# Performance work log

Hardware: AMD Instinct MI355X
Metric: run time of the kernel (lower is better)

Reference implementation:

```python
import jax, jax.numpy as jnp
import numpy as np


def _sage_layer(x, src, dst, W_self, W_neigh, b, n_nodes):
    # mean aggregation over incoming edges: agg[v] = mean(x[u] for (u,v) in E)
    agg = jax.ops.segment_sum(x[src], dst, num_segments=n_nodes)          # [N, D]
    cnt = jax.ops.segment_sum(jnp.ones((src.shape[0],), x.dtype), dst,
                              num_segments=n_nodes)                        # [N]
    agg = agg / jnp.clip(cnt, 1.0)[:, None]
    # h = ReLU(x W_self^T + agg W_neigh^T + b)   (torch Linear weight is [out, in])
    h = jnp.einsum('nd,od->no', x, W_self) + jnp.einsum('nd,od->no', agg, W_neigh) + b
    return jax.nn.relu(h)


def setup_inputs() -> dict:
    key = jax.random.key(0)
    ks = jax.random.split(key, 7)
    N, E = 50000, 800000
    F_IN, H, F_OUT = 128, 256, 128
    x = jax.random.normal(ks[0], (N, F_IN), dtype=jnp.float32)
    edge_index = jax.random.randint(ks[1], (2, E), 0, N, dtype=jnp.int64)
    s = 0.05
    return {
        'x': x,
        'edge_index': edge_index,
        'W_self1': jax.random.normal(ks[2], (H, F_IN), dtype=jnp.float32) * s,
        'W_neigh1': jax.random.normal(ks[3], (H, F_IN), dtype=jnp.float32) * s,
        'b1': jnp.zeros((H,), dtype=jnp.float32),
        'W_self2': jax.random.normal(ks[4], (F_OUT, H), dtype=jnp.float32) * s,
        'W_neigh2': jax.random.normal(ks[5], (F_OUT, H), dtype=jnp.float32) * s,
        'b2': jnp.zeros((F_OUT,), dtype=jnp.float32),
    }


def reference(x, edge_index, W_self1, W_neigh1, b1, W_self2, W_neigh2, b2):
    n_nodes = x.shape[0]
    src, dst = edge_index[0], edge_index[1]
    h = _sage_layer(x, src, dst, W_self1, W_neigh1, b1, n_nodes)
    # dropout is identity at inference
    h = _sage_layer(h, src, dst, W_self2, W_neigh2, b2, n_nodes)
    return h
```

## Files before the change

### kernel.cpp

```cpp
#include <hip/hip_runtime.h>


#define CAP 64
#define CPAD 16
#define NSLICE 8

typedef __attribute__((ext_vector_type(8))) short bfrag;
typedef __attribute__((ext_vector_type(4))) float ffrag;

__device__ inline unsigned short f2bf(float f) {
    union { float f; unsigned u; } v; v.f = f;
    unsigned r = (v.u + 0x7FFFu + ((v.u >> 16) & 1u)) >> 16;
    return (unsigned short)r;
}

__global__ __launch_bounds__(256) void prep_kernel(
        const int* __restrict__ src, const int* __restrict__ dst,
        int* __restrict__ cnt, unsigned short* __restrict__ adj,
        int E, int nper, int nfill,
        const float* __restrict__ x, unsigned short* __restrict__ xb, long xn4,
        int xblocks,
        const float* __restrict__ W0, const float* __restrict__ W1,
        const float* __restrict__ W2, const float* __restrict__ W3,
        unsigned short* __restrict__ O0, unsigned short* __restrict__ O1,
        unsigned short* __restrict__ O2, unsigned short* __restrict__ O3)
{
    int b = blockIdx.x;
    if (b < nfill) {
        int slice = b & (NSLICE - 1);
        int e = (b >> 3) * 256 + (int)threadIdx.x;
        if (e >= E) return;
        int d = dst[e];
        if ((unsigned)(d - slice * nper) >= (unsigned)nper) return;
        int s = src[e];
        int r = atomicAdd(&cnt[d * CPAD], 1);
        if (r < CAP) adj[(size_t)d * CAP + r] = (unsigned short)s;
        return;
    }
    b -= nfill;
    if (b < xblocks) {
        long i = (long)b * 256 + threadIdx.x;
        if (i >= xn4) return;
        float4 v = *(const float4*)(x + i * 4);
        ushort4 o;
        o.x = f2bf(v.x); o.y = f2bf(v.y); o.z = f2bf(v.z); o.w = f2bf(v.w);
        *(ushort4*)(xb + i * 4) = o;
        return;
    }
    b -= xblocks;
    int i = b * 256 + (int)threadIdx.x;
    int sel = i >> 13, off = i & 8191;
    const float* srcw = (sel == 0) ? W0 : (sel == 1) ? W1 : (sel == 2) ? W2 : W3;
    unsigned short* dstw = (sel == 0) ? O0 : (sel == 1) ? O1 : (sel == 2) ? O2 : O3;
    float4 v = ((const float4*)srcw)[off];
    ushort4 o;
    o.x = f2bf(v.x); o.y = f2bf(v.y); o.z = f2bf(v.z); o.w = f2bf(v.w);
    ((ushort4*)dstw)[off] = o;
}

#define BFLO(u) __uint_as_float((u) << 16)
#define BFHI(u) __uint_as_float((u) & 0xFFFF0000u)

#define ACC8(V)  do {                                                          \
    acc0 += BFLO(V.x); acc1 += BFHI(V.x); acc2 += BFLO(V.y); acc3 += BFHI(V.y);\
    acc4 += BFLO(V.z); acc5 += BFHI(V.z); acc6 += BFLO(V.w); acc7 += BFHI(V.w);\
} while (0)

__global__ __launch_bounds__(256, 2) void fused_l1(
        const unsigned short* __restrict__ xbu, const int* __restrict__ cnt,
        const unsigned short* __restrict__ adj,
        const short* __restrict__ Ws, const short* __restrict__ Wn,
        const float* __restrict__ bias, unsigned short* __restrict__ h1b, int NT)
{
    const short* xb = (const short*)xbu;
    const int wave = threadIdx.x >> 6, lane = threadIdx.x & 63;
    const int ln = lane & 15, lk = lane >> 4;
    const int gn = threadIdx.x >> 4;
    const int sp = threadIdx.x & 15;

    __shared__ unsigned short aggT[16][136];

    bfrag wfs[4][4], wfn[4][4];
    #pragma unroll
    for (int m = 0; m < 4; ++m) {
        const short* ws = Ws + (size_t)((wave * 4 + m) * 16 + ln) * 128 + lk * 8;
        const short* wn = Wn + (size_t)((wave * 4 + m) * 16 + ln) * 128 + lk * 8;
        #pragma unroll
        for (int kc = 0; kc < 4; ++kc) {
            wfs[m][kc] = *(const bfrag*)(ws + kc * 32);
            wfn[m][kc] = *(const bfrag*)(wn + kc * 32);
        }
    }
    float4 bv[4];
    #pragma unroll
    for (int m = 0; m < 4; ++m)
        bv[m] = *(const float4*)(bias + (wave * 4 + m) * 16 + lk * 4);

    for (int nt = blockIdx.x; nt < NT; nt += gridDim.x) {
        {
            int node = nt * 16 + gn;
            int c = cnt[node * CPAD]; if (c > CAP) c = CAP;
            const unsigned short* al = adj + (size_t)node * CAP;
            float acc0 = 0.f, acc1 = 0.f, acc2 = 0.f, acc3 = 0.f;
            float acc4 = 0.f, acc5 = 0.f, acc6 = 0.f, acc7 = 0.f;
            int j = 0;
            for (; j + 3 < c; j += 4) {
                ushort4 q = *(const ushort4*)(al + j);
                uint4 v0 = *(const uint4*)(xbu + (size_t)q.x * 128 + sp * 8);
                uint4 v1 = *(const uint4*)(xbu + (size_t)q.y * 128 + sp * 8);
                uint4 v2 = *(const uint4*)(xbu + (size_t)q.z * 128 + sp * 8);
                uint4 v3 = *(const uint4*)(xbu + (size_t)q.w * 128 + sp * 8);
                ACC8(v0); ACC8(v1); ACC8(v2); ACC8(v3);
            }
            for (; j < c; ++j) {
                uint4 v = *(const uint4*)(xbu + (size_t)al[j] * 128 + sp * 8);
                ACC8(v);
            }
            float s = (c > 0) ? 1.0f / (float)c : 0.0f;
            uint4 o;
            o.x = (unsigned)f2bf(acc0 * s) | ((unsigned)f2bf(acc1 * s) << 16);
            o.y = (unsigned)f2bf(acc2 * s) | ((unsigned)f2bf(acc3 * s) << 16);
            o.z = (unsigned)f2bf(acc4 * s) | ((unsigned)f2bf(acc5 * s) << 16);
            o.w = (unsigned)f2bf(acc6 * s) | ((unsigned)f2bf(acc7 * s) << 16);
            *(uint4*)(&aggT[gn][sp * 8]) = o;
        }
        __syncthreads();

        {
            const int node = nt * 16 + ln;
            bfrag nf[8];
            const short* xr = xb + (size_t)node * 128 + lk * 8;
            #pragma unroll
            for (int kc = 0; kc < 4; ++kc) {
                nf[kc]     = *(const bfrag*)(xr + kc * 32);
                nf[4 + kc] = *(const bfrag*)(&aggT[ln][lk * 8 + kc * 32]);
            }
            ffrag acc[4];
            #pragma unroll
            for (int m = 0; m < 4; ++m) {
                acc[m][0] = bv[m].x; acc[m][1] = bv[m].y;
                acc[m][2] = bv[m].z; acc[m][3] = bv[m].w;
            }
            #pragma unroll
            for (int m = 0; m < 4; ++m) {
                #pragma unroll
                for (int kc = 0; kc < 4; ++kc)
                    acc[m] = __builtin_amdgcn_mfma_f32_16x16x32_bf16(
                        wfs[m][kc], nf[kc], acc[m], 0, 0, 0);
                #pragma unroll
                for (int kc = 0; kc < 4; ++kc)
                    acc[m] = __builtin_amdgcn_mfma_f32_16x16x32_bf16(
                        wfn[m][kc], nf[4 + kc], acc[m], 0, 0, 0);
            }
            #pragma unroll
            for (int m = 0; m < 4; ++m) {
                ushort4 o;
                o.x = f2bf(fmaxf(acc[m][0], 0.f));
                o.y = f2bf(fmaxf(acc[m][1], 0.f));
                o.z = f2bf(fmaxf(acc[m][2], 0.f));
                o.w = f2bf(fmaxf(acc[m][3], 0.f));
                *(ushort4*)(h1b + (size_t)node * 256 + (wave * 4 + m) * 16 + lk * 4) = o;
            }
        }
        __syncthreads();
    }
}

__global__ __launch_bounds__(256) void gather_epilogue_bf16(
        const unsigned short* __restrict__ Zb, const unsigned short* __restrict__ S2b,
        const int* __restrict__ cnt, const unsigned short* __restrict__ adj,
        float* __restrict__ out, int N) {
    int w = (blockIdx.x * 256 + threadIdx.x) >> 6;
    int lane = threadIdx.x & 63;
    int node = w * 4 + (lane >> 4);
    int sl = lane & 15;
    if (node >= N) return;
    int c = cnt[node * CPAD]; if (c > CAP) c = CAP;
    const unsigned short* al = adj + (size_t)node * CAP;
    float acc0 = 0.f, acc1 = 0.f, acc2 = 0.f, acc3 = 0.f;
    float acc4 = 0.f, acc5 = 0.f, acc6 = 0.f, acc7 = 0.f;
    int j = 0;
    for (; j + 3 < c; j += 4) {
        ushort4 q = *(const ushort4*)(al + j);
        uint4 v0 = *(const uint4*)(Zb + (size_t)q.x * 128 + sl * 8);
        uint4 v1 = *(const uint4*)(Zb + (size_t)q.y * 128 + sl * 8);
        uint4 v2 = *(const uint4*)(Zb + (size_t)q.z * 128 + sl * 8);
        uint4 v3 = *(const uint4*)(Zb + (size_t)q.w * 128 + sl * 8);
        ACC8(v0); ACC8(v1); ACC8(v2); ACC8(v3);
    }
    for (; j < c; ++j) {
        uint4 v = *(const uint4*)(Zb + (size_t)al[j] * 128 + sl * 8);
        ACC8(v);
    }
    float s = (c > 0) ? 1.0f / (float)c : 0.0f;
    uint4 sv = *(const uint4*)(S2b + (size_t)node * 128 + sl * 8);
    float4 oa, ob;
    oa.x = fmaxf(BFLO(sv.x) + acc0 * s, 0.0f);
    oa.y = fmaxf(BFHI(sv.x) + acc1 * s, 0.0f);
    oa.z = fmaxf(BFLO(sv.y) + acc2 * s, 0.0f);
    oa.w = fmaxf(BFHI(sv.y) + acc3 * s, 0.0f);
    ob.x = fmaxf(BFLO(sv.z) + acc4 * s, 0.0f);
    ob.y = fmaxf(BFHI(sv.z) + acc5 * s, 0.0f);
    ob.z = fmaxf(BFLO(sv.w) + acc6 * s, 0.0f);
    ob.w = fmaxf(BFHI(sv.w) + acc7 * s, 0.0f);
    float* op = out + (size_t)node * 128 + sl * 8;
    *(float4*)op = oa;
    *(float4*)(op + 4) = ob;
}

#define L2_LOAD(NF, NTV) do {                                                  \
    const short* hr_ = h1b + (size_t)((NTV) * 16 + ln) * 256 + lk * 8;         \
    _Pragma("unroll") for (int kc = 0; kc < 8; ++kc)                           \
        NF[kc] = *(const bfrag*)(hr_ + kc * 32);                               \
} while (0)

#define L2_STEP(NF, CURNT) do {                                                \
    const int node_ = (CURNT) * 16 + ln;                                       \
    ffrag aS_[2], aZ_[2];                                                      \
    _Pragma("unroll") for (int m = 0; m < 2; ++m) {                            \
        aS_[m][0] = bv[m].x; aS_[m][1] = bv[m].y;                              \
        aS_[m][2] = bv[m].z; aS_[m][3] = bv[m].w;                              \
        aZ_[m][0] = 0.f; aZ_[m][1] = 0.f; aZ_[m][2] = 0.f; aZ_[m][3] = 0.f; }  \
    _Pragma("unroll") for (int m = 0; m < 2; ++m)                              \
        _Pragma("unroll") for (int kc = 0; kc < 8; ++kc) {                     \
            aS_[m] = __builtin_amdgcn_mfma_f32_16x16x32_bf16(                  \
                wfs[m][kc], NF[kc], aS_[m], 0, 0, 0);                          \
            aZ_[m] = __builtin_amdgcn_mfma_f32_16x16x32_bf16(                  \
                wfn[m][kc], NF[kc], aZ_[m], 0, 0, 0); }                        \
    _Pragma("unroll") for (int m = 0; m < 2; ++m) {                            \
        ushort4 so_;                                                           \
        so_.x = f2bf(aS_[m][0]); so_.y = f2bf(aS_[m][1]);                      \
        so_.z = f2bf(aS_[m][2]); so_.w = f2bf(aS_[m][3]);                      \
        *(ushort4*)(s2b + (size_t)node_ * 128 + (wave * 2 + m) * 16 + lk * 4) = so_; \
        ushort4 zo_;                                                           \
        zo_.x = f2bf(aZ_[m][0]); zo_.y = f2bf(aZ_[m][1]);                      \
        zo_.z = f2bf(aZ_[m][2]); zo_.w = f2bf(aZ_[m][3]);                      \
        *(ushort4*)(z2b + (size_t)node_ * 128 + (wave * 2 + m) * 16 + lk * 4) = zo_; } \
} while (0)

__global__ __launch_bounds__(256) void mfma_layer2(
        const short* __restrict__ h1b, const short* __restrict__ Ws,
        const short* __restrict__ Wn, const float* __restrict__ bias,
        unsigned short* __restrict__ s2b, unsigned short* __restrict__ z2b, int NT)
{
    const int wave = threadIdx.x >> 6, lane = threadIdx.x & 63;
    const int ln = lane & 15, lk = lane >> 4;

    bfrag wfs[2][8], wfn[2][8];
    #pragma unroll
    for (int m = 0; m < 2; ++m) {
        const short* ws = Ws + (size_t)((wave * 2 + m) * 16 + ln) * 256 + lk * 8;
        const short* wn = Wn + (size_t)((wave * 2 + m) * 16 + ln) * 256 + lk * 8;
        #pragma unroll
        for (int kc = 0; kc < 8; ++kc) {
            wfs[m][kc] = *(const bfrag*)(ws + kc * 32);
            wfn[m][kc] = *(const bfrag*)(wn + kc * 32);
        }
    }
    float4 bv[2];
    #pragma unroll
    for (int m = 0; m < 2; ++m)
        bv[m] = *(const float4*)(bias + (wave * 2 + m) * 16 + lk * 4);

    bfrag nfA[8], nfB[8];
    const int stride = gridDim.x;
    int nt = blockIdx.x;
    if (nt >= NT) return;
    L2_LOAD(nfA, nt);
    while (true) {
        int ntn = nt + stride;
        if (ntn < NT) L2_LOAD(nfB, ntn);
        L2_STEP(nfA, nt);
        nt = ntn; if (nt >= NT) break;
        ntn = nt + stride;
        if (ntn < NT) L2_LOAD(nfA, ntn);
        L2_STEP(nfB, nt);
        nt = ntn; if (nt >= NT) break;
    }
}

extern "C" void kernel_launch(void* const* d_in, const int* in_sizes, int n_in,
                              void* d_out, int out_size, void* d_ws, size_t ws_size,
                              hipStream_t stream) {
    const float* x   = (const float*)d_in[0];
    const int*   ei  = (const int*)d_in[1];
    const float* Ws1 = (const float*)d_in[2];
    const float* Wn1 = (const float*)d_in[3];
    const float* b1  = (const float*)d_in[4];
    const float* Ws2 = (const float*)d_in[5];
    const float* Wn2 = (const float*)d_in[6];
    const float* b2  = (const float*)d_in[7];
    float* out = (float*)d_out;

    const int N = in_sizes[0] / 128;
    const int E = in_sizes[1] / 2;
    const int NT = N / 16;
    const int* src = ei;
    const int* dst = ei + E;

    unsigned short* xb   = (unsigned short*)d_ws;
    unsigned short* h1b  = xb   + (size_t)N * 128;
    unsigned short* z2b  = h1b  + (size_t)N * 256;
    unsigned short* s2b  = z2b  + (size_t)N * 128;
    unsigned short* Wsb1 = s2b  + (size_t)N * 128;
    unsigned short* Wnb1 = Wsb1 + 32768;
    unsigned short* Wsb2 = Wnb1 + 32768;
    unsigned short* Wnb2 = Wsb2 + 32768;
    int* cnt = (int*)(Wnb2 + 32768);
    unsigned short* adj = (unsigned short*)(cnt + (size_t)N * CPAD);

    const int nper    = (N + NSLICE - 1) / NSLICE;
    const int nfill   = ((E + 255) / 256) * NSLICE;
    const long xn4    = (long)N * 128 / 4;
    const int xblocks = (int)((xn4 + 255) / 256);
    const int prep_blocks = nfill + xblocks + 128;

    hipMemsetAsync(cnt, 0, (size_t)N * CPAD * sizeof(int), stream);
    prep_kernel<<<prep_blocks, 256, 0, stream>>>(
        src, dst, cnt, adj, E, nper, nfill,
        x, xb, xn4, xblocks,
        Ws1, Wn1, Ws2, Wn2, Wsb1, Wnb1, Wsb2, Wnb2);

    fused_l1<<<512, 256, 0, stream>>>(
        xb, cnt, adj, (const short*)Wsb1, (const short*)Wnb1, b1, h1b, NT);

    mfma_layer2<<<512, 256, 0, stream>>>(
        (const short*)h1b, (const short*)Wsb2, (const short*)Wnb2, b2, s2b, z2b, NT);
    gather_epilogue_bf16<<<(N * 16 + 255) / 256, 256, 0, stream>>>(
        z2b, s2b, cnt, adj, out, N);
}
```

Measured before the change: 242.2 us.

## Bucket edges by destination slice before building adjacency lists

The old adjacency fill had each edge block re-read all edges once per slice (8x redundant reads). Now a first kernel reads each edge once and appends a packed dst/src word to a per-slice buffer, using block-local counting and one global atomic per slice. A second kernel walks each slice buffer and does the per-node atomic insert, so that slice's writes stay localized. It also adds empty asm constraints to keep weight fragments resident in registers inside fused_l1. This costs an extra launch, extra workspace and a fixed per-slice capacity that could overflow on skewed inputs.

```diff
diff --git a/kernel.cpp b/kernel.cpp
--- a/kernel.cpp
+++ b/kernel.cpp
@@ -4,6 +4,7 @@
 #define CAP 64
 #define CPAD 16
 #define NSLICE 8
+#define SLCAP 131072
 
 typedef __attribute__((ext_vector_type(8))) short bfrag;
 typedef __attribute__((ext_vector_type(4))) float ffrag;
@@ -14,10 +15,10 @@
     return (unsigned short)r;
 }
 
-__global__ __launch_bounds__(256) void prep_kernel(
+__global__ __launch_bounds__(256) void prep_a(
         const int* __restrict__ src, const int* __restrict__ dst,
-        int* __restrict__ cnt, unsigned short* __restrict__ adj,
-        int E, int nper, int nfill,
+        int* __restrict__ gcnt, unsigned* __restrict__ slicebuf,
+        int E, int nper, int nfillA,
         const float* __restrict__ x, unsigned short* __restrict__ xb, long xn4,
         int xblocks,
         const float* __restrict__ W0, const float* __restrict__ W1,
@@ -26,18 +27,39 @@
         unsigned short* __restrict__ O2, unsigned short* __restrict__ O3)
 {
     int b = blockIdx.x;
-    if (b < nfill) {
-        int slice = b & (NSLICE - 1);
-        int e = (b >> 3) * 256 + (int)threadIdx.x;
-        if (e >= E) return;
-        int d = dst[e];
-        if ((unsigned)(d - slice * nper) >= (unsigned)nper) return;
-        int s = src[e];
-        int r = atomicAdd(&cnt[d * CPAD], 1);
-        if (r < CAP) adj[(size_t)d * CAP + r] = (unsigned short)s;
+    if (b < nfillA) {
+        __shared__ int cntL[NSLICE];
+        __shared__ int baseG[NSLICE];
+        if (threadIdx.x < NSLICE) cntL[threadIdx.x] = 0;
+        __syncthreads();
+        int e0 = b * 1024 + (int)threadIdx.x * 4;
+        int dv[4], sv[4], sl[4], rk[4];
+        bool val[4];
+        #pragma unroll
+        for (int k = 0; k < 4; ++k) {
+            int e = e0 + k;
+            val[k] = e < E;
+            dv[k] = val[k] ? dst[e] : 0;
+            sv[k] = val[k] ? src[e] : 0;
+            sl[k] = (int)((unsigned)dv[k] / (unsigned)nper);
+            if (val[k]) rk[k] = atomicAdd(&cntL[sl[k]], 1);
+        }
+        __syncthreads();
+        if (threadIdx.x < NSLICE)
+            baseG[threadIdx.x] = atomicAdd(&gcnt[threadIdx.x * 16], cntL[threadIdx.x]);
+        __syncthreads();
+        #pragma unroll
+        for (int k = 0; k < 4; ++k) {
+            if (val[k]) {
+                int pos = baseG[sl[k]] + rk[k];
+                if (pos < SLCAP)
+                    slicebuf[(size_t)sl[k] * SLCAP + pos] =
+                        ((unsigned)dv[k] << 16) | (unsigned)sv[k];
+            }
+        }
         return;
     }
-    b -= nfill;
+    b -= nfillA;
     if (b < xblocks) {
         long i = (long)b * 256 + threadIdx.x;
         if (i >= xn4) return;
@@ -58,6 +80,22 @@
     ((ushort4*)dstw)[off] = o;
 }
 
+__global__ __launch_bounds__(256) void prep_b(
+        const unsigned* __restrict__ slicebuf, const int* __restrict__ gcnt,
+        int* __restrict__ cnt, unsigned short* __restrict__ adj)
+{
+    int slice = blockIdx.x & (NSLICE - 1);
+    int n = gcnt[slice * 16]; if (n > SLCAP) n = SLCAP;
+    const unsigned* sb = slicebuf + (size_t)slice * SLCAP;
+    int stride = (gridDim.x >> 3) * 256;
+    for (int i = (blockIdx.x >> 3) * 256 + (int)threadIdx.x; i < n; i += stride) {
+        unsigned v = sb[i];
+        int d = (int)(v >> 16), s = (int)(v & 0xFFFFu);
+        int r = atomicAdd(&cnt[d * CPAD], 1);
+        if (r < CAP) adj[(size_t)d * CAP + r] = (unsigned short)s;
+    }
+}
+
 #define BFLO(u) __uint_as_float((u) << 16)
 #define BFHI(u) __uint_as_float((u) & 0xFFFF0000u)
 
@@ -65,6 +103,8 @@
     acc0 += BFLO(V.x); acc1 += BFHI(V.x); acc2 += BFLO(V.y); acc3 += BFHI(V.y);\
     acc4 += BFLO(V.z); acc5 += BFHI(V.z); acc6 += BFLO(V.w); acc7 += BFHI(V.w);\
 } while (0)
+
+#define PIN4(a, b, c, d) asm volatile("" : "+v"(a), "+v"(b), "+v"(c), "+v"(d))
 
 __global__ __launch_bounds__(256, 2) void fused_l1(
         const unsigned short* __restrict__ xbu, const int* __restrict__ cnt,
@@ -97,6 +137,15 @@
         bv[m] = *(const float4*)(bias + (wave * 4 + m) * 16 + lk * 4);
 
     for (int nt = blockIdx.x; nt < NT; nt += gridDim.x) {
+        PIN4(wfs[0][0], wfs[0][1], wfs[0][2], wfs[0][3]);
+        PIN4(wfs[1][0], wfs[1][1], wfs[1][2], wfs[1][3]);
+        PIN4(wfs[2][0], wfs[2][1], wfs[2][2], wfs[2][3]);
+        PIN4(wfs[3][0], wfs[3][1], wfs[3][2], wfs[3][3]);
+        PIN4(wfn[0][0], wfn[0][1], wfn[0][2], wfn[0][3]);
+        PIN4(wfn[1][0], wfn[1][1], wfn[1][2], wfn[1][3]);
+        PIN4(wfn[2][0], wfn[2][1], wfn[2][2], wfn[2][3]);
+        PIN4(wfn[3][0], wfn[3][1], wfn[3][2], wfn[3][3]);
+
         {
             int node = nt * 16 + gn;
             int c = cnt[node * CPAD]; if (c > CAP) c = CAP;
@@ -306,20 +355,25 @@
     unsigned short* Wnb1 = Wsb1 + 32768;
     unsigned short* Wsb2 = Wnb1 + 32768;
     unsigned short* Wnb2 = Wsb2 + 32768;
-    int* cnt = (int*)(Wnb2 + 32768);
-    unsigned short* adj = (unsigned short*)(cnt + (size_t)N * CPAD);
+    int* cnt    = (int*)(Wnb2 + 32768);
+    int* gcnt   = cnt + (size_t)N * CPAD;
+    unsigned short* adj = (unsigned short*)(gcnt + NSLICE * 16);
+    unsigned* slicebuf  = (unsigned*)(adj + (size_t)N * CAP);
 
     const int nper    = (N + NSLICE - 1) / NSLICE;
-    const int nfill   = ((E + 255) / 256) * NSLICE;
+    const int nfillA  = (E + 1023) / 1024;
     const long xn4    = (long)N * 128 / 4;
     const int xblocks = (int)((xn4 + 255) / 256);
-    const int prep_blocks = nfill + xblocks + 128;
-
-    hipMemsetAsync(cnt, 0, (size_t)N * CPAD * sizeof(int), stream);
-    prep_kernel<<<prep_blocks, 256, 0, stream>>>(
-        src, dst, cnt, adj, E, nper, nfill,
+    const int prep_blocks = nfillA + xblocks + 128;
+
+    hipMemsetAsync(cnt, 0, ((size_t)N * CPAD + NSLICE * 16) * sizeof(int), stream);
+
+    prep_a<<<prep_blocks, 256, 0, stream>>>(
+        src, dst, gcnt, slicebuf, E, nper, nfillA,
         x, xb, xn4, xblocks,
         Ws1, Wn1, Ws2, Wn2, Wsb1, Wnb1, Wsb2, Wnb2);
+
+    prep_b<<<512, 256, 0, stream>>>(slicebuf, gcnt, cnt, adj);
 
     fused_l1<<<512, 256, 0, stream>>>(
         xb, cnt, adj, (const short*)Wsb1, (const short*)Wnb1, b1, h1b, NT);
```

After: 259.4 us. +7.1%, slower.
